# Performance work log

Hardware: AMD Instinct MI355X
Metric: run time of the kernel (lower is better)

Reference implementation:

```python
import jax, jax.numpy as jnp
import numpy as np
import math

B, D, E = 32768, 256, 8          # batch, feature dim (shape=[256]), num_steps experts
T_TOTAL = 1.0
H_STEP = T_TOTAL / E             # self.h
EIGMIN, EIGINIT, EIGMAX = -1.0, 0.0, 1.0
LOGIT_099 = math.log(0.99 / 0.01)


def setup_inputs() -> dict:
    key = jax.random.key(0)
    k_t, k_y, k_w1, k_w2 = jax.random.split(key, 4)
    std = 1.0 / math.sqrt(D)     # xavier-ish init for expert weights
    return {
        "t": jax.random.uniform(k_t, (B,), dtype=jnp.float32),            # times in [0, T)
        "y": jax.random.normal(k_y, (B, D), dtype=jnp.float32),
        "W1": jax.random.normal(k_w1, (E, D, D), dtype=jnp.float32) * std,
        "b1": jnp.zeros((E, D), dtype=jnp.float32),
        "W2": jax.random.normal(k_w2, (E, D, D), dtype=jnp.float32) * std,
        "b2": jnp.zeros((E, D), dtype=jnp.float32),
        "scales": jnp.full((1, D), LOGIT_099, dtype=jnp.float32),         # learn_scales=False init
        "shifta": jnp.asarray(LOGIT_099, dtype=jnp.float32),
        "shiftb": jnp.asarray(LOGIT_099, dtype=jnp.float32),
    }


def reference(t, y, W1, b1, W2, b2, scales, shifta, shiftb):
    # t2ind: clamp(int(t / h), max=E-1)
    ind = jnp.minimum((t / H_STEP).astype(jnp.int32), E - 1)            # [B]
    # per-sample dispatch to expert F[i] (2-layer MLP), grouped as masked
    # dense batched GEMMs per expert (E is a small fixed set)
    f = jnp.zeros_like(y)
    for e in range(E):
        h_e = jnp.tanh(jnp.einsum('bd,kd->bk', y, W1[e]) + b1[e])       # [B, D]
        f_e = jnp.einsum('bd,kd->bk', h_e, W2[e]) + b2[e]               # [B, D]
        f = jnp.where((ind == e)[:, None], f_e, f)
    # sigmoid-scale / affine-combine epilogue
    f = jax.nn.sigmoid(scales) * f
    a = EIGINIT + jax.nn.sigmoid(shifta) * (EIGMIN - EIGINIT)
    b = EIGINIT + jax.nn.sigmoid(shiftb) * (EIGMAX - EIGINIT)
    return 0.5 * ((b - a) * f + (a + b) * y)
```

## Files before the change

kernel.cpp:

```cpp
#include <hip/hip_runtime.h>

#define BATCH 32768
#define DIM   256
#define NEXP  8
#define MT    64
#define STRIDE 264

typedef __bf16 bf16x8 __attribute__((ext_vector_type(8)));
typedef __bf16 bf16x4 __attribute__((ext_vector_type(4)));
typedef float  f32x16 __attribute__((ext_vector_type(16)));

static __device__ __forceinline__ float sigmoid_f(float x) {
    return __builtin_amdgcn_rcpf(1.f + __expf(-x));
}
static __device__ __forceinline__ float tanh_f(float x) {
    return 1.f - 2.f * __builtin_amdgcn_rcpf(__expf(2.f * x) + 1.f);
}

__global__ void prep_kernel(const float* __restrict__ W1, const float* __restrict__ W2,
                            const float* __restrict__ t,
                            bf16x8* __restrict__ W1p, bf16x8* __restrict__ W2p,
                            int* __restrict__ cursor, int* __restrict__ idxb) {
    const int b = blockIdx.x;
    if (b < 256) {
        const int tid = b * 256 + threadIdx.x;
        const int kh  = tid & 1;
        const int ks  = (tid >> 1) & 15;
        const int col = (tid >> 5) & 255;
        const int e   = tid >> 13;
        const long src = (long)tid * 8;
        const float4 a0 = *(const float4*)(W1 + src);
        const float4 a1 = *(const float4*)(W1 + src + 4);
        const float4 c0 = *(const float4*)(W2 + src);
        const float4 c1 = *(const float4*)(W2 + src + 4);
        bf16x8 w1, w2;
        w1[0] = (__bf16)a0.x; w1[1] = (__bf16)a0.y; w1[2] = (__bf16)a0.z; w1[3] = (__bf16)a0.w;
        w1[4] = (__bf16)a1.x; w1[5] = (__bf16)a1.y; w1[6] = (__bf16)a1.z; w1[7] = (__bf16)a1.w;
        w2[0] = (__bf16)c0.x; w2[1] = (__bf16)c0.y; w2[2] = (__bf16)c0.z; w2[3] = (__bf16)c0.w;
        w2[4] = (__bf16)c1.x; w2[5] = (__bf16)c1.y; w2[6] = (__bf16)c1.z; w2[7] = (__bf16)c1.w;
        const int dst = (e << 13) | ((col >> 5) << 10) | (ks << 6) | (kh << 5) | (col & 31);
        W1p[dst] = w1;
        W2p[dst] = w2;
    } else {
        __shared__ int h[NEXP], base[NEXP];
        if (threadIdx.x < NEXP) h[threadIdx.x] = 0;
        __syncthreads();
        const int i = (b - 256) * 256 + threadIdx.x;
        const int e = min((int)(t[i] * 8.0f), NEXP - 1);
        const int lr = atomicAdd(&h[e], 1);
        __syncthreads();
        if (threadIdx.x < NEXP)
            base[threadIdx.x] = atomicAdd(&cursor[threadIdx.x], h[threadIdx.x]);
        __syncthreads();
        idxb[e * BATCH + base[e] + lr] = i;
    }
}

__global__ void __launch_bounds__(512, 4)
mlp_kernel(const float* __restrict__ y,
           const float* __restrict__ scales,
           const float* __restrict__ shifta,
           const float* __restrict__ shiftb,
           const float* __restrict__ b1,
           const float* __restrict__ b2,
           const bf16x8* __restrict__ W1p,
           const bf16x8* __restrict__ W2p,
           const int* __restrict__ cnt,
           const int* __restrict__ idxb,
           float* __restrict__ out) {
    __shared__ __bf16 ab[MT * STRIDE];
    __shared__ int rows[MT];

    const int tx   = threadIdx.x;
    const int wave = tx >> 6;
    const int lane = tx & 63;
    const int nl   = lane & 31;
    const int kh   = lane >> 5;
    const int ncol = wave * 32;

    int c[NEXP], tp[NEXP + 1];
    tp[0] = 0;
#pragma unroll
    for (int e = 0; e < NEXP; ++e) {
        c[e] = cnt[e];
        tp[e + 1] = tp[e] + ((c[e] + MT - 1) >> 6);
    }
    const int total = tp[NEXP];

    const float sa = sigmoid_f(shifta[0]);
    const float sb = sigmoid_f(shiftb[0]);
    const float av = -sa;
    const float bvv = sb;
    const float k1 = 0.5f * (bvv - av);
    const float k2 = 0.5f * (av + bvv);
    const bool needy = (k2 != 0.0f);

    for (int tile = blockIdx.x; tile < total; tile += gridDim.x) {
        int e = 0;
#pragma unroll
        for (int j = 0; j < NEXP; ++j) if (tile >= tp[j + 1]) e = j + 1;
        const int rbase = (tile - tp[e]) * MT;
        const int nrows = min(MT, c[e] - rbase);
        const int* idx_e = idxb + e * BATCH;

        __syncthreads();
#pragma unroll
        for (int pass = 0; pass < 8; ++pass) {
            const int r  = pass * 8 + wave;
            const int rr = min(r, nrows - 1);
            const int g  = idx_e[rbase + rr];
            if (lane == 0) rows[r] = (r < nrows) ? g : -1;
            const float4 v = *(const float4*)(y + (long)g * DIM + lane * 4);
            bf16x4 w;
            w[0] = (__bf16)v.x; w[1] = (__bf16)v.y; w[2] = (__bf16)v.z; w[3] = (__bf16)v.w;
            *(bf16x4*)(ab + r * STRIDE + lane * 4) = w;
        }
        __syncthreads();

        const __bf16* apt0 = ab + nl * STRIDE + kh * 8;
        const __bf16* apt1 = ab + (32 + nl) * STRIDE + kh * 8;

        const bf16x8* w1p = W1p + (e << 13) + (wave << 10) + lane;
        f32x16 acc[2] = {};
#pragma unroll
        for (int ks = 0; ks < 16; ++ks) {
            bf16x8 a0 = *(const bf16x8*)(apt0 + ks * 16);
            bf16x8 a1 = *(const bf16x8*)(apt1 + ks * 16);
            bf16x8 bb = w1p[ks << 6];
            acc[0] = __builtin_amdgcn_mfma_f32_32x32x16_bf16(a0, bb, acc[0], 0, 0, 0);
            acc[1] = __builtin_amdgcn_mfma_f32_32x32x16_bf16(a1, bb, acc[1], 0, 0, 0);
        }
        __syncthreads();

        {
            const int n = ncol + nl;
            const float b1v = b1[(e << 8) | n];
#pragma unroll
            for (int mi = 0; mi < 2; ++mi) {
#pragma unroll
                for (int r = 0; r < 16; ++r) {
                    const int row = mi * 32 + (r & 3) + ((r >> 2) << 3) + (kh << 2);
                    ab[row * STRIDE + n] = (__bf16)tanh_f(acc[mi][r] + b1v);
                }
            }
        }
        __syncthreads();

        const bf16x8* w2p = W2p + (e << 13) + (wave << 10) + lane;
        f32x16 acc2[2] = {};
#pragma unroll
        for (int ks = 0; ks < 16; ++ks) {
            bf16x8 a0 = *(const bf16x8*)(apt0 + ks * 16);
            bf16x8 a1 = *(const bf16x8*)(apt1 + ks * 16);
            bf16x8 bb = w2p[ks << 6];
            acc2[0] = __builtin_amdgcn_mfma_f32_32x32x16_bf16(a0, bb, acc2[0], 0, 0, 0);
            acc2[1] = __builtin_amdgcn_mfma_f32_32x32x16_bf16(a1, bb, acc2[1], 0, 0, 0);
        }

        {
            const int n = ncol + nl;
            const float c1  = k1 * sigmoid_f(scales[n]);
            const float b2v = b2[(e << 8) | n];
#pragma unroll
            for (int mi = 0; mi < 2; ++mi) {
#pragma unroll
                for (int r = 0; r < 16; ++r) {
                    const int row = mi * 32 + (r & 3) + ((r >> 2) << 3) + (kh << 2);
                    const int g = rows[row];
                    if (g >= 0) {
                        float res = c1 * (acc2[mi][r] + b2v);
                        if (needy) res += k2 * y[(long)g * DIM + n];
                        out[(long)g * DIM + n] = res;
                    }
                }
            }
        }
    }
}

extern "C" void kernel_launch(void* const* d_in, const int* in_sizes, int n_in,
                              void* d_out, int out_size, void* d_ws, size_t ws_size,
                              hipStream_t stream) {
    const float* t      = (const float*)d_in[0];
    const float* y      = (const float*)d_in[1];
    const float* W1     = (const float*)d_in[2];
    const float* b1     = (const float*)d_in[3];
    const float* W2     = (const float*)d_in[4];
    const float* b2     = (const float*)d_in[5];
    const float* scales = (const float*)d_in[6];
    const float* shifta = (const float*)d_in[7];
    const float* shiftb = (const float*)d_in[8];
    float* out = (float*)d_out;

    char* ws = (char*)d_ws;
    int* cursor = (int*)ws;
    int* idxb   = (int*)(ws + 256);
    bf16x8* W1p = (bf16x8*)(ws + 256 + NEXP * BATCH * 4);
    bf16x8* W2p = W1p + 65536;

    hipMemsetAsync(cursor, 0, 32, stream);
    prep_kernel<<<384, 256, 0, stream>>>(W1, W2, t, W1p, W2p, cursor, idxb);
    mlp_kernel<<<520, 512, 0, stream>>>(y, scales, shifta, shiftb, b1, b2,
                                        W1p, W2p, cursor, idxb, out);
}
```

Baseline: 133.4 us.

## Prefetch next tile's activations into registers during current tile's GEMMs

Restructures the persistent tile loop so that the row indices and y rows of the next tile are loaded into registers while the current tile runs its two MFMA GEMMs and epilogues. After the current tile finishes, the prefetched values are converted to bf16 and written to shared memory. The grid shrinks from 520 to 256 blocks and launch bounds drop to 2 waves per SIMD, leaving more registers for the prefetch buffers. The aim is to hide global gather latency, at the cost of register pressure and lower occupancy, and roughly 16 blocks of tiles per block may leave load imbalance.

After: 145.5 us. 1.09x slower.

```diff
diff --git a/kernel.cpp b/kernel.cpp
--- a/kernel.cpp
+++ b/kernel.cpp
@@ -5,6 +5,7 @@
 #define NEXP  8
 #define MT    64
 #define STRIDE 264
+#define GRID  256
 
 typedef __bf16 bf16x8 __attribute__((ext_vector_type(8)));
 typedef __bf16 bf16x4 __attribute__((ext_vector_type(4)));
@@ -56,7 +57,7 @@
     }
 }
 
-__global__ void __launch_bounds__(512, 4)
+__global__ void __launch_bounds__(512, 2)
 mlp_kernel(const float* __restrict__ y,
            const float* __restrict__ scales,
            const float* __restrict__ shifta,
@@ -95,15 +96,19 @@
     const float k2 = 0.5f * (av + bvv);
     const bool needy = (k2 != 0.0f);
 
-    for (int tile = blockIdx.x; tile < total; tile += gridDim.x) {
-        int e = 0;
+    int tile = blockIdx.x;
+    if (tile >= total) return;
+
+    int e = 0, rbase, nrows;
+    {
 #pragma unroll
         for (int j = 0; j < NEXP; ++j) if (tile >= tp[j + 1]) e = j + 1;
-        const int rbase = (tile - tp[e]) * MT;
-        const int nrows = min(MT, c[e] - rbase);
+        rbase = (tile - tp[e]) * MT;
+        nrows = min(MT, c[e] - rbase);
+    }
+
+    {
         const int* idx_e = idxb + e * BATCH;
-
-        __syncthreads();
 #pragma unroll
         for (int pass = 0; pass < 8; ++pass) {
             const int r  = pass * 8 + wave;
@@ -115,7 +120,31 @@
             w[0] = (__bf16)v.x; w[1] = (__bf16)v.y; w[2] = (__bf16)v.z; w[3] = (__bf16)v.w;
             *(bf16x4*)(ab + r * STRIDE + lane * 4) = w;
         }
-        __syncthreads();
+    }
+    __syncthreads();
+
+    for (;;) {
+        const int ntile = tile + GRID;
+        const bool have_next = (ntile < total);
+        int e2 = 0, rbase2 = 0, nrows2 = 0;
+        int g2[8];
+        float4 v2[8];
+        if (have_next) {
+#pragma unroll
+            for (int j = 0; j < NEXP; ++j) if (ntile >= tp[j + 1]) e2 = j + 1;
+            rbase2 = (ntile - tp[e2]) * MT;
+            nrows2 = min(MT, c[e2] - rbase2);
+            const int* idx2 = idxb + e2 * BATCH;
+#pragma unroll
+            for (int pass = 0; pass < 8; ++pass) {
+                const int r  = pass * 8 + wave;
+                const int rr = min(r, nrows2 - 1);
+                g2[pass] = idx2[rbase2 + rr];
+            }
+#pragma unroll
+            for (int pass = 0; pass < 8; ++pass)
+                v2[pass] = *(const float4*)(y + (long)g2[pass] * DIM + lane * 4);
+        }
 
         const __bf16* apt0 = ab + nl * STRIDE + kh * 8;
         const __bf16* apt1 = ab + (32 + nl) * STRIDE + kh * 8;
@@ -175,6 +204,23 @@
                 }
             }
         }
+
+        if (!have_next) return;
+
+        __syncthreads();
+
+#pragma unroll
+        for (int pass = 0; pass < 8; ++pass) {
+            const int r = pass * 8 + wave;
+            if (lane == 0) rows[r] = (r < nrows2) ? g2[pass] : -1;
+            const float4 v = v2[pass];
+            bf16x4 w;
+            w[0] = (__bf16)v.x; w[1] = (__bf16)v.y; w[2] = (__bf16)v.z; w[3] = (__bf16)v.w;
+            *(bf16x4*)(ab + r * STRIDE + lane * 4) = w;
+        }
+        __syncthreads();
+
+        tile = ntile; e = e2; rbase = rbase2; nrows = nrows2;
     }
 }
 
@@ -200,6 +246,6 @@
 
     hipMemsetAsync(cursor, 0, 32, stream);
     prep_kernel<<<384, 256, 0, stream>>>(W1, W2, t, W1p, W2p, cursor, idxb);
-    mlp_kernel<<<520, 512, 0, stream>>>(y, scales, shifta, shiftb, b1, b2,
-                                        W1p, W2p, cursor, idxb, out);
-}
+    mlp_kernel<<<GRID, 512, 0, stream>>>(y, scales, shifta, shiftb, b1, b2,
+                                         W1p, W2p, cursor, idxb, out);
+}
```
